# Optimization experiments

Measured on AMD Instinct MI355X. Metric: run time of the kernel, lower is better.

Reference implementation:

```python
import jax, jax.numpy as jnp
import numpy as np

# NVFP4 (e2m1) 4-bit codebook: sign bit in the high position of the nibble
_NVFP4_CODE = jnp.array([0.0, 0.5, 1.0, 1.5, 2.0, 3.0, 4.0, 6.0,
                         -0.0, -0.5, -1.0, -1.5, -2.0, -3.0, -4.0, -6.0],
                        dtype=jnp.float32)

M = 4096          # tokens (batch*seq)
K = 4096          # in_features
N_NVFP4 = 2048
N_FP8 = 1024
N_FP16 = 1024
N = N_NVFP4 + N_FP8 + N_FP16  # out_features
BLOCK = 16        # NVFP4 scale block size along K


def setup_inputs() -> dict:
    key = jax.random.key(0)
    ks = jax.random.split(key, 8)
    x = jax.random.normal(ks[0], (M, K), dtype=jnp.float32)
    nvfp4_idx = jax.random.randint(ks[1], (N_NVFP4, K), 0, 16, dtype=jnp.int32)
    nvfp4_scales = jax.random.uniform(ks[2], (N_NVFP4, K // BLOCK), dtype=jnp.float32) * 0.5 + 0.05
    nvfp4_global_scale = jax.random.uniform(ks[3], (1,), dtype=jnp.float32) * 0.5 + 0.5
    w_fp8 = jax.random.normal(ks[4], (N_FP8, K), dtype=jnp.float32)
    fp8_scale = jax.random.uniform(ks[5], (1,), dtype=jnp.float32) * 0.1 + 0.01
    w_fp16 = jax.random.normal(ks[6], (N_FP16, K), dtype=jnp.float32) * 0.02
    bias = jax.random.normal(ks[7], (N,), dtype=jnp.float32) * 0.01
    inv_perm = jax.random.permutation(jax.random.fold_in(key, 99), N).astype(jnp.int64)
    return {"x": x, "nvfp4_idx": nvfp4_idx, "nvfp4_scales": nvfp4_scales,
            "nvfp4_global_scale": nvfp4_global_scale, "w_fp8": w_fp8,
            "fp8_scale": fp8_scale, "w_fp16": w_fp16, "bias": bias,
            "inv_perm": inv_perm}


def reference(x, nvfp4_idx, nvfp4_scales, nvfp4_global_scale,
              w_fp8, fp8_scale, w_fp16, bias, inv_perm):
    # --- NVFP4 group: dequantize 4-bit codes with per-16-block fp8 scales + global scale
    codes = _NVFP4_CODE[nvfp4_idx]                                   # [n_nvfp4, K]
    scales_full = jnp.repeat(nvfp4_scales, BLOCK, axis=1)            # [n_nvfp4, K]
    w_nvfp4 = codes * scales_full * nvfp4_global_scale[0]            # [n_nvfp4, K]
    y_nvfp4 = jnp.einsum('mk,nk->mn', x, w_nvfp4)                    # [M, n_nvfp4]
    # --- FP8 group: per-tensor scale
    y_fp8 = jnp.einsum('mk,nk->mn', x, w_fp8) * fp8_scale[0]         # [M, n_fp8]
    # --- FP16 group: plain GEMM
    y_fp16 = jnp.einsum('mk,nk->mn', x, w_fp16)                      # [M, n_fp16]
    # --- Reassemble in original channel order via inverse permutation
    y_grouped = jnp.concatenate([y_nvfp4, y_fp8, y_fp16], axis=-1)   # [M, N]
    y = jnp.take(y_grouped, inv_perm, axis=-1)
    return y + bias
```

## Files before the change

kernel.cpp:

```cpp
#include <hip/hip_runtime.h>

#define M_DIM 4096
#define N_DIM 4096
#define K_DIM 4096

typedef float f32x4 __attribute__((ext_vector_type(4)));
typedef __bf16 bf16x8 __attribute__((ext_vector_type(8)));

__device__ __forceinline__ unsigned short f2b(float f) {
    unsigned int u = __float_as_uint(f);
    u += 0x7fffu + ((u >> 16) & 1u);
    return (unsigned short)(u >> 16);
}

__device__ __forceinline__ float nvfp4_decode(int n) {
    unsigned m = (unsigned)n & 7u;
    unsigned e = m >> 1, f = m & 1u;
    unsigned bits = (m >= 2u) ? (((126u + e) << 23) | (f << 22))
                              : (m * 0x3f000000u);
    bits |= ((unsigned)n & 8u) << 28;
    return __uint_as_float(bits);
}

__global__ __launch_bounds__(256) void xconv_kernel(
        const float* __restrict__ x, unsigned short* __restrict__ xb) {
    size_t i = ((size_t)blockIdx.x * 256 + threadIdx.x) * 8;
    float4 a0 = *(const float4*)(x + i);
    float4 a1 = *(const float4*)(x + i + 4);
    union { unsigned short h[8]; uint4 u; } o;
    o.h[0] = f2b(a0.x); o.h[1] = f2b(a0.y); o.h[2] = f2b(a0.z); o.h[3] = f2b(a0.w);
    o.h[4] = f2b(a1.x); o.h[5] = f2b(a1.y); o.h[6] = f2b(a1.z); o.h[7] = f2b(a1.w);
    *(uint4*)(xb + i) = o.u;
}

__global__ __launch_bounds__(256) void wbuild_kernel(
        const int* __restrict__ idx4, const float* __restrict__ sc4,
        const float* __restrict__ gs4, const float* __restrict__ w8,
        const float* __restrict__ s8, const float* __restrict__ w16,
        const int* __restrict__ iperm, unsigned short* __restrict__ W) {
    const int j = blockIdx.x;
    const int t = threadIdx.x;
    const int g = iperm[j];

#pragma unroll
    for (int h = 0; h < 2; ++h) {
        const int k0 = h * 2048 + t * 8;
        union { unsigned short hh[8]; uint4 u; } o;
        if (g < 2048) {
            const float s = sc4[(size_t)g * (K_DIM / 16) + (k0 >> 4)] * gs4[0];
            const int4* ip = (const int4*)(idx4 + (size_t)g * K_DIM + k0);
            int4 v0 = ip[0], v1 = ip[1];
            o.hh[0] = f2b(nvfp4_decode(v0.x) * s);
            o.hh[1] = f2b(nvfp4_decode(v0.y) * s);
            o.hh[2] = f2b(nvfp4_decode(v0.z) * s);
            o.hh[3] = f2b(nvfp4_decode(v0.w) * s);
            o.hh[4] = f2b(nvfp4_decode(v1.x) * s);
            o.hh[5] = f2b(nvfp4_decode(v1.y) * s);
            o.hh[6] = f2b(nvfp4_decode(v1.z) * s);
            o.hh[7] = f2b(nvfp4_decode(v1.w) * s);
        } else if (g < 3072) {
            const float s = s8[0];
            const float4* wp = (const float4*)(w8 + (size_t)(g - 2048) * K_DIM + k0);
            float4 v0 = wp[0], v1 = wp[1];
            o.hh[0] = f2b(v0.x * s); o.hh[1] = f2b(v0.y * s);
            o.hh[2] = f2b(v0.z * s); o.hh[3] = f2b(v0.w * s);
            o.hh[4] = f2b(v1.x * s); o.hh[5] = f2b(v1.y * s);
            o.hh[6] = f2b(v1.z * s); o.hh[7] = f2b(v1.w * s);
        } else {
            const float4* wp = (const float4*)(w16 + (size_t)(g - 3072) * K_DIM + k0);
            float4 v0 = wp[0], v1 = wp[1];
            o.hh[0] = f2b(v0.x); o.hh[1] = f2b(v0.y);
            o.hh[2] = f2b(v0.z); o.hh[3] = f2b(v0.w);
            o.hh[4] = f2b(v1.x); o.hh[5] = f2b(v1.y);
            o.hh[6] = f2b(v1.z); o.hh[7] = f2b(v1.w);
        }
        *(uint4*)(W + (size_t)j * K_DIM + k0) = o.u;
    }
}

#define GLOAD_LDS16(g, l)                                                     \
    __builtin_amdgcn_global_load_lds(                                         \
        (const __attribute__((address_space(1))) void*)(unsigned long long)(g),\
        (__attribute__((address_space(3))) void*)(unsigned int)(unsigned long long)(l), \
        16, 0, 0)

#define STAGE(p, d, kt, buf) do {                                             \
    const unsigned short* _s = (p) + (size_t)(kt) * 64;                       \
    GLOAD_LDS16(_s,      smem + (buf) * 32768 + (d));                         \
    GLOAD_LDS16(_s + 32, smem + (buf) * 32768 + (d) + 1024);                  \
} while (0)

#define LOADA(AF, buf, qm) do {                                               \
    _Pragma("unroll") for (int mi = 0; mi < 4; ++mi)                          \
        _Pragma("unroll") for (int kk = 0; kk < 2; ++kk)                      \
            AF[mi][kk] = *(const bf16x8*)(rdA + (buf) * 32768 +               \
                                          (((qm) * 8 + mi * 2 + kk) << 10));  \
} while (0)

#define LOADB(buf, qn) do {                                                   \
    _Pragma("unroll") for (int nj = 0; nj < 2; ++nj)                          \
        _Pragma("unroll") for (int kk = 0; kk < 2; ++kk)                      \
            bq[nj][kk] = *(const bf16x8*)(rdB + (buf) * 32768 +               \
                                          (((qn) * 4 + nj * 2 + kk) << 10));  \
} while (0)

#define MMA(AF, qm, qn) do {                                                  \
    _Pragma("unroll") for (int mi = 0; mi < 4; ++mi)                          \
        _Pragma("unroll") for (int nj = 0; nj < 2; ++nj) {                    \
            acc[(qm)*4+mi][(qn)*2+nj] = __builtin_amdgcn_mfma_f32_16x16x32_bf16( \
                AF[mi][0], bq[nj][0], acc[(qm)*4+mi][(qn)*2+nj], 0, 0, 0);    \
            acc[(qm)*4+mi][(qn)*2+nj] = __builtin_amdgcn_mfma_f32_16x16x32_bf16( \
                AF[mi][1], bq[nj][1], acc[(qm)*4+mi][(qn)*2+nj], 0, 0, 0);    \
        }                                                                     \
} while (0)

#define BARRIER __builtin_amdgcn_s_barrier()
#define WAIT_LGKM asm volatile("s_waitcnt lgkmcnt(0)" ::: "memory")
#define WAIT_VM4 asm volatile("s_waitcnt vmcnt(4)" ::: "memory")
#define PRIO1 __builtin_amdgcn_s_setprio(1)
#define PRIO0 __builtin_amdgcn_s_setprio(0)

__global__ __launch_bounds__(512, 2) void gemm_kernel(
        const unsigned short* __restrict__ X, const unsigned short* __restrict__ W,
        const float* __restrict__ bias, float* __restrict__ C) {
    __shared__ __align__(128) unsigned char smem[131072];

    const int pid = blockIdx.x;
    const int wg = (pid & 7) * 32 + (pid >> 3);
    const int bm = wg >> 4, bn = wg & 15;
    const int m0 = bm * 256, n0 = bn * 256;

    const int tid  = threadIdx.x;
    const int wave = tid >> 6;
    const int lane = tid & 63;
    const int wr   = wave >> 2;
    const int wc   = wave & 3;
    const int l16  = lane & 15;
    const int quad = lane >> 4;

    const int srow = lane >> 2;
    const int scol = ((lane & 3) ^ ((lane >> 5) << 1)) << 3;

    const unsigned short* pA0 = X + (size_t)(m0 + (wr * 8 + wc) * 16 + srow) * K_DIM + scol;
    const unsigned short* pA1 = pA0 + (size_t)64 * K_DIM;
    const unsigned short* pB0 = W + (size_t)(n0 + (wc * 4 + wr) * 16 + srow) * K_DIM + scol;
    const unsigned short* pB1 = pB0 + (size_t)32 * K_DIM;

    const int dA0 = (((wr * 8 + wc) * 2) << 10) + lane * 16;
    const int dA1 = dA0 + 8192;
    const int dB0 = 65536 + (((wc * 4 + wr) * 2) << 10) + lane * 16;
    const int dB1 = dB0 + 4096;

    const int inner_rd = ((l16 << 6) | (quad << 4)) ^ ((l16 & 8) << 2);
    const unsigned char* rdA = smem + ((wr * 16) << 10) + inner_rd;
    const unsigned char* rdB = smem + 65536 + ((wc * 8) << 10) + inner_rd;

    f32x4 acc[8][4] = {};
    bf16x8 af0[4][2], af1[4][2], bq[2][2];

    STAGE(pA0, dA0, 0, 0);
    STAGE(pB0, dB0, 0, 0);
    STAGE(pB1, dB1, 0, 0);
    STAGE(pA1, dA1, 0, 0);
    STAGE(pA0, dA0, 1, 1);
    STAGE(pB1, dB1, 1, 1);
    WAIT_VM4;
    BARRIER;

#pragma unroll 1
    for (int it = 0; it < 32; ++it) {
        const int t1 = 2 * it + 1;
        const int t2 = (2 * it + 2) & 63;
        const int t3 = (2 * it + 3) & 63;

        LOADA(af0, 0, 0); LOADB(0, 0);
        STAGE(pB0, dB0, t1, 1);
        BARRIER; WAIT_LGKM;
        PRIO1; MMA(af0, 0, 0); PRIO0;
        BARRIER;
        LOADA(af1, 0, 1);
        STAGE(pA1, dA1, t1, 1);
        BARRIER; WAIT_LGKM;
        PRIO1; MMA(af1, 1, 0); PRIO0;
        BARRIER;
        LOADB(0, 1);
        STAGE(pA0, dA0, t2, 0);
        BARRIER; WAIT_LGKM;
        PRIO1; MMA(af1, 1, 1); PRIO0;
        BARRIER;
        STAGE(pB1, dB1, t2, 0);
        BARRIER;
        PRIO1; MMA(af0, 0, 1); PRIO0;
        WAIT_VM4;
        BARRIER;

        LOADA(af0, 1, 0); LOADB(1, 0);
        STAGE(pB0, dB0, t2, 0);
        BARRIER; WAIT_LGKM;
        PRIO1; MMA(af0, 0, 0); PRIO0;
        BARRIER;
        LOADA(af1, 1, 1);
        STAGE(pA1, dA1, t2, 0);
        BARRIER; WAIT_LGKM;
        PRIO1; MMA(af1, 1, 0); PRIO0;
        BARRIER;
        LOADB(1, 1);
        STAGE(pA0, dA0, t3, 1);
        BARRIER; WAIT_LGKM;
        PRIO1; MMA(af1, 1, 1); PRIO0;
        BARRIER;
        STAGE(pB1, dB1, t3, 1);
        BARRIER;
        PRIO1; MMA(af0, 0, 1); PRIO0;
        WAIT_VM4;
        BARRIER;
    }

    const int crow0 = m0 + wr * 128 + quad * 4;
    const int ccol0 = n0 + wc * 64 + l16;
    float bv[4];
#pragma unroll
    for (int p = 0; p < 4; ++p) bv[p] = bias[ccol0 + p * 16];
#pragma unroll
    for (int q = 0; q < 8; ++q) {
#pragma unroll
        for (int p = 0; p < 4; ++p) {
            const int col = ccol0 + p * 16;
            const int row = crow0 + q * 16;
#pragma unroll
            for (int r = 0; r < 4; ++r)
                C[(size_t)(row + r) * N_DIM + col] = acc[q][p][r] + bv[p];
        }
    }
}

extern "C" void kernel_launch(void* const* d_in, const int* in_sizes, int n_in,
                              void* d_out, int out_size, void* d_ws, size_t ws_size,
                              hipStream_t stream) {
    const float* x            = (const float*)d_in[0];
    const int*   nvfp4_idx    = (const int*)d_in[1];
    const float* nvfp4_scales = (const float*)d_in[2];
    const float* gscale       = (const float*)d_in[3];
    const float* w_fp8        = (const float*)d_in[4];
    const float* fp8_scale    = (const float*)d_in[5];
    const float* w_fp16       = (const float*)d_in[6];
    const float* bias         = (const float*)d_in[7];
    const int*   inv_perm     = (const int*)d_in[8];
    float* out = (float*)d_out;

    unsigned short* xb = (unsigned short*)d_ws;
    unsigned short* wb = xb + (size_t)M_DIM * K_DIM;

    xconv_kernel<<<8192, 256, 0, stream>>>(x, xb);
    wbuild_kernel<<<4096, 256, 0, stream>>>(nvfp4_idx, nvfp4_scales, gscale,
                                            w_fp8, fp8_scale, w_fp16,
                                            inv_perm, wb);
    gemm_kernel<<<256, 512, 0, stream>>>(xb, wb, bias, out);
}
```

Measured before the change: 293.9 us.

## Replace fine-grained 8-wave ping-pong schedule with simple double-buffered K-tile loop

Replaces the interleaved schedule, which issued partial global stages between MMA quarters with many barriers and lgkm waits, with a plain double-buffered loop. Each K-tile now issues all four global-to-LDS stages for the next tile, loads fragments from the current buffer, runs the MMAs, then waits on vmcnt(0) and a single barrier. A sched_barrier fence keeps the compiler from moving instructions across tile boundaries. This cuts barrier count and lets the compiler schedule LDS reads against MFMAs, but it gives up the finer overlap, and the full vmcnt(0) wait exposes global-load latency at the end of every tile.

```diff
diff --git a/kernel.cpp b/kernel.cpp
--- a/kernel.cpp
+++ b/kernel.cpp
@@ -115,10 +115,28 @@
 } while (0)
 
 #define BARRIER __builtin_amdgcn_s_barrier()
-#define WAIT_LGKM asm volatile("s_waitcnt lgkmcnt(0)" ::: "memory")
-#define WAIT_VM4 asm volatile("s_waitcnt vmcnt(4)" ::: "memory")
+#define WAIT_VM0 asm volatile("s_waitcnt vmcnt(0)" ::: "memory")
+#define SCHED_FENCE __builtin_amdgcn_sched_barrier(0)
 #define PRIO1 __builtin_amdgcn_s_setprio(1)
 #define PRIO0 __builtin_amdgcn_s_setprio(0)
+
+#define KTILE(buf, tn) do {                                                   \
+    STAGE(pA0, dA0, (tn), (buf) ^ 1);                                         \
+    STAGE(pB0, dB0, (tn), (buf) ^ 1);                                         \
+    STAGE(pA1, dA1, (tn), (buf) ^ 1);                                         \
+    STAGE(pB1, dB1, (tn), (buf) ^ 1);                                         \
+    LOADB((buf), 0);                                                          \
+    LOADA(af0, (buf), 0);                                                     \
+    LOADA(af1, (buf), 1);                                                     \
+    PRIO1; MMA(af0, 0, 0); PRIO0;                                             \
+    PRIO1; MMA(af1, 1, 0); PRIO0;                                             \
+    LOADB((buf), 1);                                                          \
+    PRIO1; MMA(af1, 1, 1); PRIO0;                                             \
+    PRIO1; MMA(af0, 0, 1); PRIO0;                                             \
+    WAIT_VM0;                                                                 \
+    BARRIER;                                                                  \
+    SCHED_FENCE;                                                              \
+} while (0)
 
 __global__ __launch_bounds__(512, 2) void gemm_kernel(
         const unsigned short* __restrict__ X, const unsigned short* __restrict__ W,
@@ -160,60 +178,18 @@
 
     STAGE(pA0, dA0, 0, 0);
     STAGE(pB0, dB0, 0, 0);
+    STAGE(pA1, dA1, 0, 0);
     STAGE(pB1, dB1, 0, 0);
-    STAGE(pA1, dA1, 0, 0);
-    STAGE(pA0, dA0, 1, 1);
-    STAGE(pB1, dB1, 1, 1);
-    WAIT_VM4;
+    WAIT_VM0;
     BARRIER;
+    SCHED_FENCE;
 
 #pragma unroll 1
-    for (int it = 0; it < 32; ++it) {
-        const int t1 = 2 * it + 1;
-        const int t2 = (2 * it + 2) & 63;
-        const int t3 = (2 * it + 3) & 63;
-
-        LOADA(af0, 0, 0); LOADB(0, 0);
-        STAGE(pB0, dB0, t1, 1);
-        BARRIER; WAIT_LGKM;
-        PRIO1; MMA(af0, 0, 0); PRIO0;
-        BARRIER;
-        LOADA(af1, 0, 1);
-        STAGE(pA1, dA1, t1, 1);
-        BARRIER; WAIT_LGKM;
-        PRIO1; MMA(af1, 1, 0); PRIO0;
-        BARRIER;
-        LOADB(0, 1);
-        STAGE(pA0, dA0, t2, 0);
-        BARRIER; WAIT_LGKM;
-        PRIO1; MMA(af1, 1, 1); PRIO0;
-        BARRIER;
-        STAGE(pB1, dB1, t2, 0);
-        BARRIER;
-        PRIO1; MMA(af0, 0, 1); PRIO0;
-        WAIT_VM4;
-        BARRIER;
-
-        LOADA(af0, 1, 0); LOADB(1, 0);
-        STAGE(pB0, dB0, t2, 0);
-        BARRIER; WAIT_LGKM;
-        PRIO1; MMA(af0, 0, 0); PRIO0;
-        BARRIER;
-        LOADA(af1, 1, 1);
-        STAGE(pA1, dA1, t2, 0);
-        BARRIER; WAIT_LGKM;
-        PRIO1; MMA(af1, 1, 0); PRIO0;
-        BARRIER;
-        LOADB(1, 1);
-        STAGE(pA0, dA0, t3, 1);
-        BARRIER; WAIT_LGKM;
-        PRIO1; MMA(af1, 1, 1); PRIO0;
-        BARRIER;
-        STAGE(pB1, dB1, t3, 1);
-        BARRIER;
-        PRIO1; MMA(af0, 0, 1); PRIO0;
-        WAIT_VM4;
-        BARRIER;
+    for (int it2 = 0; it2 < 32; ++it2) {
+        const int ta = 2 * it2 + 1;
+        const int tb = (2 * it2 + 2) & 63;
+        KTILE(0, ta);
+        KTILE(1, tb);
     }
 
     const int crow0 = m0 + wr * 128 + quad * 4;
```

After: 293.7 us. Within noise of the previous version (-0.1%).
